# Performance work log

Hardware: AMD Instinct MI355X
Metric: run time of the kernel (lower is better)

The kernel has to match this reference:

```python
import jax, jax.numpy as jnp
import numpy as np

TOP_K = 64
TEMPERATURE = 1.0
EPS = 1e-12  # torch F.normalize eps


def _normalize(v):
    # matches torch.nn.functional.normalize(v, dim=-1)
    n = jnp.linalg.norm(v, axis=-1, keepdims=True)
    return v / jnp.maximum(n, EPS)


def setup_inputs() -> dict:
    key = jax.random.key(0)
    k1, k2 = jax.random.split(key)
    x = jax.random.normal(k1, (4, 1024, 768), dtype=jnp.float32)
    codebook = jax.random.normal(k2, (8192, 768), dtype=jnp.float32)
    alpha = jnp.float32(0.5)
    return {"x": x, "codebook": codebook, "alpha": alpha}


def reference(x, codebook, alpha):
    K = TOP_K
    x_n = _normalize(x)                              # [B,T,D]
    cb_n = _normalize(codebook)                      # [N,D]
    sims = jnp.einsum('btd,nd->btn', x_n, cb_n)      # [B,T,N]
    activations = jax.nn.relu(sims)
    topk_vals, topk_idx = jax.lax.top_k(activations, K)  # [B,T,K]
    protos = codebook[topk_idx]                      # [B,T,K,D] gather
    protos_n = _normalize(protos)
    # per-token KxK pairwise similarity
    sim = jnp.einsum('btkd,btjd->btkj', protos_n, protos_n)
    sim = sim - jnp.eye(K, dtype=sim.dtype)
    sim = jax.nn.relu(sim)
    w = jax.nn.softmax(topk_vals / TEMPERATURE, axis=-1)  # [B,T,K]
    inhibition = jnp.einsum('btkj,btj->btk', sim, w)      # [B,T,K]
    result_topk = jax.nn.relu(topk_vals * (1.0 - alpha * inhibition))
    out = jnp.einsum('btk,btkd->btd', result_topk, protos)  # weighted sum
    return x + out
```

## Files before the change

kernel.cpp:

```cpp
#include <hip/hip_runtime.h>

#define TOKENS 4096
#define DIM    768
#define NCODE  8192
#define TOPK   64
#define CAP    384
#define LCAP   24
#define TAU    0.07f
#define NBIN   256
#define SELCAP 128
#define POOL   80
#define BLO    61
#define BHI    67

typedef __attribute__((ext_vector_type(4))) float          f32x4;
typedef __attribute__((ext_vector_type(8))) _Float16       half8;
typedef __attribute__((ext_vector_type(8))) unsigned short ushort8;
typedef __attribute__((ext_vector_type(16))) signed char   c8x16;
typedef __attribute__((ext_vector_type(8)))  signed char   c8x8;

__device__ __forceinline__ unsigned short f2h(float f) {
  _Float16 h = (_Float16)f;
  return *(unsigned short*)&h;
}
__device__ __forceinline__ float h2f(unsigned short u) {
  _Float16 h = *(_Float16*)&u;
  return (float)h;
}

__device__ __forceinline__ int binof(float v) {
  int b = (int)((v - TAU) * (256.0f / 0.28f));
  return b < 0 ? 0 : (b > 255 ? 255 : b);
}

__device__ __forceinline__ void gload16(const unsigned short* g, unsigned short* l) {
  __builtin_amdgcn_global_load_lds((const __attribute__((address_space(1))) unsigned int*)g,
                                   (__attribute__((address_space(3))) unsigned int*)l,
                                   16, 0, 0);
}

__device__ __forceinline__ double dot12(const float4& xa, const float4& xb, const float4& xc,
                                        const float4& a, const float4& b, const float4& c) {
  double acc = (double)xa.x * (double)a.x;
  acc = fma((double)xa.y, (double)a.y, acc);
  acc = fma((double)xa.z, (double)a.z, acc);
  acc = fma((double)xa.w, (double)a.w, acc);
  acc = fma((double)xb.x, (double)b.x, acc);
  acc = fma((double)xb.y, (double)b.y, acc);
  acc = fma((double)xb.z, (double)b.z, acc);
  acc = fma((double)xb.w, (double)b.w, acc);
  acc = fma((double)xc.x, (double)c.x, acc);
  acc = fma((double)xc.y, (double)c.y, acc);
  acc = fma((double)xc.z, (double)c.z, acc);
  acc = fma((double)xc.w, (double)c.w, acc);
  return acc;
}

__global__ __launch_bounds__(256) void normcvt_kernel(const float* __restrict__ X,
                                                      const float* __restrict__ CB,
                                                      unsigned short* __restrict__ Xn,
                                                      unsigned short* __restrict__ CBn,
                                                      signed char* __restrict__ CBq,
                                                      float* __restrict__ scs,
                                                      double* __restrict__ rxd,
                                                      double* __restrict__ rcd) {
  int row = blockIdx.x, tid = threadIdx.x;
  bool isCB = row >= TOKENS;
  int lrow = isCB ? row - TOKENS : row;
  const float* v = (isCB ? CB : X) + (size_t)lrow * DIM;
  float a = v[tid], b = v[tid + 256], c = v[tid + 512];
  double s = (double)a * a + (double)b * b + (double)c * c;
#pragma unroll
  for (int off = 32; off > 0; off >>= 1) s += __shfl_xor(s, off);
  __shared__ double red[4];
  __shared__ float s_rf, s_qs;
  __shared__ float redm[4];
  if ((tid & 63) == 0) red[tid >> 6] = s;
  __syncthreads();
  if (tid == 0) {
    double t = red[0] + red[1] + red[2] + red[3];
    double r = 1.0 / fmax(sqrt(t), 1e-12);
    (isCB ? rcd : rxd)[lrow] = r;
    s_rf = (float)r;
  }
  __syncthreads();
  float rf = s_rf;
  float na = a * rf, nb = b * rf, nc = c * rf;
  unsigned short* o = (isCB ? CBn : Xn) + (size_t)lrow * DIM;
  o[tid]       = f2h(na);
  o[tid + 256] = f2h(nb);
  o[tid + 512] = f2h(nc);
  if (isCB) {
    float m = fmaxf(fabsf(na), fmaxf(fabsf(nb), fabsf(nc)));
#pragma unroll
    for (int off = 32; off > 0; off >>= 1) m = fmaxf(m, __shfl_xor(m, off));
    if ((tid & 63) == 0) redm[tid >> 6] = m;
    __syncthreads();
    if (tid == 0) {
      float M = fmaxf(fmaxf(redm[0], redm[1]), fmaxf(redm[2], redm[3]));
      M = fmaxf(M, 1e-8f);
      s_qs = 127.0f / M;
      scs[lrow] = M / 127.0f;
    }
    __syncthreads();
    float qs = s_qs;
    signed char* q = CBq + (size_t)lrow * DIM;
    int qa = (int)rintf(na * qs); qa = qa > 127 ? 127 : (qa < -127 ? -127 : qa);
    int qb = (int)rintf(nb * qs); qb = qb > 127 ? 127 : (qb < -127 ? -127 : qb);
    int qc = (int)rintf(nc * qs); qc = qc > 127 ? 127 : (qc < -127 ? -127 : qc);
    q[tid]       = (signed char)qa;
    q[tid + 256] = (signed char)qb;
    q[tid + 512] = (signed char)qc;
  }
}

__global__ __launch_bounds__(256, 4) void cand_gemm(const unsigned short* __restrict__ Xn,
                                                    const unsigned short* __restrict__ CBn,
                                                    int* __restrict__ cnt,
                                                    float* __restrict__ cval,
                                                    unsigned short* __restrict__ cidx) {
  __shared__ __attribute__((aligned(16))) unsigned short As[2][128 * 32];
  __shared__ __attribute__((aligned(16))) unsigned short Bs[2][128 * 32];
  int tid = threadIdx.x;

  int bid = blockIdx.x;
  int xcd = bid & 7;
  int pos = bid >> 3;
  int sr  = pos >> 6;
  int rr  = pos & 63;
  int mt  = sr * 8 + (rr & 7);
  int nt  = xcd * 8 + (rr >> 3);
  int bm = mt * 128, bn = nt * 128;

  int wave = tid >> 6, lane = tid & 63;
  int wm = (wave >> 1) * 64, wn = (wave & 1) * 64;
  int col = lane & 15, q = lane >> 4;

  int scol = (((lane & 3) ^ ((lane >> 2) & 3)) * 8);
  const unsigned short* gA0 = Xn  + (size_t)(bm + wave * 32 + (lane >> 2)) * DIM + scol;
  const unsigned short* gB0 = CBn + (size_t)(bn + wave * 32 + (lane >> 2)) * DIM + scol;
  int lofs = wave * 32 * 32;

  f32x4 acc[4][4];
#pragma unroll
  for (int mi = 0; mi < 4; ++mi)
#pragma unroll
    for (int ni = 0; ni < 4; ++ni) acc[mi][ni] = (f32x4){0.f, 0.f, 0.f, 0.f};

#pragma unroll
  for (int j = 0; j < 2; ++j) {
    gload16(gA0 + (size_t)(j * 16) * DIM, &As[0][lofs + j * 16 * 32]);
    gload16(gB0 + (size_t)(j * 16) * DIM, &Bs[0][lofs + j * 16 * 32]);
  }

  int rsw = (q ^ (col & 3)) * 8;
  for (int it = 0; it < 24; ++it) {
    int cur = it & 1, nxt = cur ^ 1;
    __syncthreads();
    if (it < 23) {
      int k1 = (it + 1) * 32;
#pragma unroll
      for (int j = 0; j < 2; ++j) {
        gload16(gA0 + (size_t)(j * 16) * DIM + k1, &As[nxt][lofs + j * 16 * 32]);
        gload16(gB0 + (size_t)(j * 16) * DIM + k1, &Bs[nxt][lofs + j * 16 * 32]);
      }
    }
    half8 af[4], bf[4];
#pragma unroll
    for (int mi = 0; mi < 4; ++mi)
      af[mi] = *(const half8*)&As[cur][(wm + mi * 16 + col) * 32 + rsw];
#pragma unroll
    for (int ni = 0; ni < 4; ++ni)
      bf[ni] = *(const half8*)&Bs[cur][(wn + ni * 16 + col) * 32 + rsw];
#pragma unroll
    for (int mi = 0; mi < 4; ++mi)
#pragma unroll
      for (int ni = 0; ni < 4; ++ni)
        acc[mi][ni] = __builtin_amdgcn_mfma_f32_16x16x32_f16(af[mi], bf[ni], acc[mi][ni], 0, 0, 0);
  }
  __syncthreads();

  float* lv            = (float*)&As[0][0];
  unsigned short* lid  = (unsigned short*)&Bs[0][0];
  int* lcnt            = (int*)((char*)&Bs[0][0] + 128 * LCAP * 2);
  int* lbase           = lcnt + 128;
  if (tid < 128) lcnt[tid] = 0;
  __syncthreads();
#pragma unroll
  for (int mi = 0; mi < 4; ++mi)
#pragma unroll
    for (int rg = 0; rg < 4; ++rg) {
      int ml = wm + mi * 16 + q * 4 + rg;
#pragma unroll
      for (int ni = 0; ni < 4; ++ni) {
        float val = acc[mi][ni][rg];
        if (val > TAU) {
          int n = bn + wn + ni * 16 + col;
          int s = atomicAdd(&lcnt[ml], 1);
          if (s < LCAP) { lv[ml * LCAP + s] = val; lid[ml * LCAP + s] = (unsigned short)n; }
        }
      }
    }
  __syncthreads();

  if (tid < 128) {
    int c = lcnt[tid]; c = c < LCAP ? c : LCAP;
    lcnt[tid] = c;
    lbase[tid] = atomicAdd(&cnt[bm + tid], c);
  }
  __syncthreads();
  {
    int ml = tid >> 1, half = tid & 1;
    int c = lcnt[ml], base = lbase[ml], m = bm + ml;
    for (int s = half; s < c; s += 2) {
      int g = base + s;
      if (g < CAP) {
        cval[(size_t)m * CAP + g] = lv[ml * LCAP + s];
        cidx[(size_t)m * CAP + g] = lid[ml * LCAP + s];
      }
    }
  }
}

__global__ __launch_bounds__(128) void select_kernel(const float* __restrict__ X,
                                                     const float* __restrict__ CB,
                                                     const double* __restrict__ rxd,
                                                     const double* __restrict__ rcd,
                                                     const int* __restrict__ cnt,
                                                     const float* __restrict__ cval,
                                                     const unsigned short* __restrict__ cidx,
                                                     unsigned short* __restrict__ gidx,
                                                     float* __restrict__ gvals) {
  int t = blockIdx.x, tid = threadIdx.x;
  int wave = tid >> 6, lane = tid & 63;

  __shared__ float  s_cv[CAP];
  __shared__ int    s_cid[CAP];
  __shared__ int    hist[NBIN];
  __shared__ float  s_selv[SELCAP];
  __shared__ int    s_seli[SELCAP];
  __shared__ float  s_ordv[POOL];
  __shared__ int    s_ord[POOL];
  __shared__ double s_bex[BHI - BLO];
  __shared__ int    s_idx[64];
  __shared__ float  s_vals[64];
  __shared__ int    s_n, s_pivot;

  int c = cnt[t]; c = c < CAP ? c : CAP;
  for (int s = tid; s < c; s += 128) {
    s_cv[s]  = cval[(size_t)t * CAP + s];
    s_cid[s] = (int)cidx[(size_t)t * CAP + s];
  }
  hist[tid] = 0;
  hist[tid + 128] = 0;
  if (tid == 0) s_n = 0;
  __syncthreads();
  for (int s = tid; s < c; s += 128) atomicAdd(&hist[binof(s_cv[s])], 1);
  __syncthreads();

  int target = c < POOL ? c : POOL;
  if (wave == 0) {
    int h0 = hist[4 * lane], h1 = hist[4 * lane + 1], h2 = hist[4 * lane + 2], h3 = hist[4 * lane + 3];
    int T = h0 + h1 + h2 + h3;
#pragma unroll
    for (int off = 1; off < 64; off <<= 1) {
      int x = __shfl_down(T, off);
      T += (lane + off < 64) ? x : 0;
    }
    int s0 = T, s1 = T - h0, s2 = s1 - h1, s3 = s2 - h2;
    int bk = -1;
    if (s3 >= target) bk = 3;
    else if (s2 >= target) bk = 2;
    else if (s1 >= target) bk = 1;
    else if (s0 >= target) bk = 0;
    unsigned long long m = __ballot(bk >= 0);
    int hl = 63 - __builtin_clzll(m);
    if (lane == hl) s_pivot = 4 * lane + bk;
  }
  __syncthreads();
  int pivot = s_pivot;
  for (int s = tid; s < c; s += 128) {
    if (binof(s_cv[s]) >= pivot) {
      int p = atomicAdd(&s_n, 1);
      if (p < SELCAP) { s_selv[p] = s_cv[s]; s_seli[p] = s_cid[s]; }
    }
  }
  __syncthreads();
  int nsel = s_n < SELCAP ? s_n : SELCAP;

  if (tid < nsel) {
    float vi = s_selv[tid]; int ci = s_seli[tid];
    int rank = 0;
    for (int j = 0; j < nsel; ++j) {
      float vj = s_selv[j]; int cj = s_seli[j];
      rank += (vj > vi || (vj == vi && cj < ci)) ? 1 : 0;
    }
    if (rank < POOL) { s_ord[rank] = ci; s_ordv[rank] = vi; }
  }
  if (tid < 64) { s_vals[tid] = 0.0f; s_idx[tid] = 0; }
  __syncthreads();

  int nord = nsel < POOL ? nsel : POOL;
  int lo = nord < BLO ? nord : BLO;
  int hi = nord < BHI ? nord : BHI;
  int B  = hi - lo;

  float4 xa = *(const float4*)(X + (size_t)t * DIM + 4 * lane);
  float4 xb = *(const float4*)(X + (size_t)t * DIM + 256 + 4 * lane);
  float4 xc = *(const float4*)(X + (size_t)t * DIM + 512 + 4 * lane);
  double rxt = rxd[t];
  for (int j = wave * 2; j < B; j += 4) {
    int r1ok = (j + 1) < B;
    int gi0 = s_ord[lo + j];
    int gi1 = r1ok ? s_ord[lo + j + 1] : gi0;
    const float* p0 = CB + (size_t)gi0 * DIM;
    const float* p1 = CB + (size_t)gi1 * DIM;
    float4 a0 = *(const float4*)(p0 + 4 * lane);
    float4 b0 = *(const float4*)(p0 + 256 + 4 * lane);
    float4 c0 = *(const float4*)(p0 + 512 + 4 * lane);
    float4 a1 = *(const float4*)(p1 + 4 * lane);
    float4 b1 = *(const float4*)(p1 + 256 + 4 * lane);
    float4 c1 = *(const float4*)(p1 + 512 + 4 * lane);
    double acc0 = dot12(xa, xb, xc, a0, b0, c0);
    double acc1 = dot12(xa, xb, xc, a1, b1, c1);
#pragma unroll
    for (int off = 32; off > 0; off >>= 1) {
      acc0 += __shfl_xor(acc0, off);
      acc1 += __shfl_xor(acc1, off);
    }
    if (lane == 0) {
      double v0 = acc0 * rxt * rcd[gi0];
      s_bex[j] = v0 > 0.0 ? v0 : 0.0;
      if (r1ok) {
        double v1 = acc1 * rxt * rcd[gi1];
        s_bex[j + 1] = v1 > 0.0 ? v1 : 0.0;
      }
    }
  }
  __syncthreads();

  if (tid < lo) { s_idx[tid] = s_ord[tid]; s_vals[tid] = s_ordv[tid]; }
  if (tid < B) {
    double vi = s_bex[tid]; int ci = s_ord[lo + tid];
    int rb = 0;
    for (int j = 0; j < B; ++j) {
      double vj = s_bex[j]; int cj = s_ord[lo + j];
      rb += (vj > vi || (vj == vi && cj < ci)) ? 1 : 0;
    }
    int slot = lo + rb;
    if (slot < TOPK) { s_idx[slot] = ci; s_vals[slot] = (float)vi; }
  }
  __syncthreads();

  if (tid < 64) {
    gidx[(size_t)t * 64 + tid]  = (unsigned short)s_idx[tid];
    gvals[(size_t)t * 64 + tid] = s_vals[tid];
  }
}

__global__ __launch_bounds__(256) void gram_kernel(const float* __restrict__ X,
                                                   const signed char* __restrict__ CBq,
                                                   const float* __restrict__ scs,
                                                   const double* __restrict__ rcd,
                                                   const unsigned short* __restrict__ gidx,
                                                   const float* __restrict__ gvals,
                                                   const float* __restrict__ alpha_p,
                                                   float* __restrict__ OUT) {
  int t = blockIdx.x, tid = threadIdx.x;
  int wave = tid >> 6, lane = tid & 63;

  __shared__ __attribute__((aligned(16))) unsigned char u_mem[17408];
  unsigned short (*Pb)[136] = (unsigned short (*)[136])u_mem;

  __shared__ int   s_idx[64];
  __shared__ float s_vals[64], s_w[64], s_rn[64], s_res[64];

  if (tid < 64) {
    s_idx[tid]  = (int)gidx[(size_t)t * 64 + tid];
    s_vals[tid] = gvals[(size_t)t * 64 + tid];
  }
  __syncthreads();

  if (tid < 64) {
    float v = s_vals[tid];
    float m = v;
#pragma unroll
    for (int off = 32; off > 0; off >>= 1) m = fmaxf(m, __shfl_xor(m, off));
    float e = expf(v - m);
    float se = e;
#pragma unroll
    for (int off = 32; off > 0; off >>= 1) se += __shfl_xor(se, off);
    s_w[tid] = e / se;
  }

  int q = lane >> 4, col = lane & 15;
  int frow = wave * 16 + col;
  int kof  = q * 8;
  f32x4 gacc[4];
#pragma unroll
  for (int cj = 0; cj < 4; ++cj) gacc[cj] = (f32x4){0.f, 0.f, 0.f, 0.f};
  int r = tid >> 2, qq = tid & 3;
  const signed char* Pg = CBq + (size_t)s_idx[r] * DIM;
  c8x16 stq[2];
  stq[0] = *(const c8x16*)(Pg + qq * 32);
  stq[1] = *(const c8x16*)(Pg + qq * 32 + 16);
  for (int cch = 0; cch < 6; ++cch) {
    if (cch) __syncthreads();
#pragma unroll
    for (int j = 0; j < 4; ++j) {
      ushort8 w;
#pragma unroll
      for (int e = 0; e < 8; ++e) w[e] = f2h((float)stq[j >> 1][(j & 1) * 8 + e]);
      *(ushort8*)&Pb[r][qq * 32 + j * 8] = w;
    }
    __syncthreads();
    if (cch < 5) {
      stq[0] = *(const c8x16*)(Pg + (cch + 1) * 128 + qq * 32);
      stq[1] = *(const c8x16*)(Pg + (cch + 1) * 128 + qq * 32 + 16);
    }
#pragma unroll
    for (int ks = 0; ks < 4; ++ks) {
      half8 a = *(const half8*)&Pb[frow][ks * 32 + kof];
#pragma unroll
      for (int cj = 0; cj < 4; ++cj) {
        half8 b = *(const half8*)&Pb[cj * 16 + col][ks * 32 + kof];
        gacc[cj] = __builtin_amdgcn_mfma_f32_16x16x32_f16(a, b, gacc[cj], 0, 0, 0);
      }
    }
  }

#pragma unroll
  for (int cj = 0; cj < 4; ++cj) {
    if (cj == wave) {
#pragma unroll
      for (int rg = 0; rg < 4; ++rg) {
        if (col == q * 4 + rg)
          s_rn[wave * 16 + q * 4 + rg] =
              1.0f / fmaxf(sqrtf(fmaxf(gacc[cj][rg], 0.0f)), 1e-12f);
      }
    }
  }
  __syncthreads();

  float alpha = alpha_p[0];
  {
    float inh[4] = {0.f, 0.f, 0.f, 0.f};
#pragma unroll
    for (int rg = 0; rg < 4; ++rg) {
      int i = wave * 16 + q * 4 + rg;
      float rni = s_rn[i];
#pragma unroll
      for (int cj = 0; cj < 4; ++cj) {
        int jcol = cj * 16 + col;
        if (jcol != i) {
          float sim = fmaxf(gacc[cj][rg] * rni * s_rn[jcol], 0.0f);
          inh[rg] += sim * s_w[jcol];
        }
      }
    }
#pragma unroll
    for (int off = 1; off < 16; off <<= 1) {
#pragma unroll
      for (int rg = 0; rg < 4; ++rg) inh[rg] += __shfl_xor(inh[rg], off);
    }
    if (col == 0) {
#pragma unroll
      for (int rg = 0; rg < 4; ++rg) {
        int i = wave * 16 + q * 4 + rg;
        int gi = s_idx[i];
        float res = s_vals[i] * (1.0f - alpha * inh[rg]);
        s_res[i] = fmaxf(res, 0.0f) * scs[gi] * (float)(1.0 / rcd[gi]);
      }
    }
  }
  __syncthreads();

  float* s_o  = (float*)u_mem;
  float* s_p1 = s_o + DIM;
  {
    float o8[8];
#pragma unroll
    for (int j = 0; j < 8; ++j) o8[j] = 0.f;
    int wr = tid / 96, wc = tid - wr * 96;
    if (wr < 2) {
      const int d8 = wc * 8;
#pragma unroll 8
      for (int i = 0; i < 32; ++i) {
        int k = 2 * i + wr;
        float rk = s_res[k];
        const signed char* p = CBq + (size_t)s_idx[k] * DIM + d8;
        c8x8 v = *(const c8x8*)p;
#pragma unroll
        for (int j = 0; j < 8; ++j) o8[j] += rk * (float)v[j];
      }
    }
    if (wr == 1) {
#pragma unroll
      for (int j = 0; j < 8; ++j) s_p1[wc * 8 + j] = o8[j];
    }
    __syncthreads();
    if (wr == 0) {
#pragma unroll
      for (int j = 0; j < 8; ++j) s_o[wc * 8 + j] = o8[j] + s_p1[wc * 8 + j];
    }
    __syncthreads();
  }

  OUT[(size_t)t * DIM + tid]       = X[(size_t)t * DIM + tid]       + s_o[tid];
  OUT[(size_t)t * DIM + tid + 256] = X[(size_t)t * DIM + tid + 256] + s_o[tid + 256];
  OUT[(size_t)t * DIM + tid + 512] = X[(size_t)t * DIM + tid + 512] + s_o[tid + 512];
}

extern "C" void kernel_launch(void* const* d_in, const int* in_sizes, int n_in,
                              void* d_out, int out_size, void* d_ws, size_t ws_size,
                              hipStream_t stream) {
  const float* X       = (const float*)d_in[0];
  const float* CB      = (const float*)d_in[1];
  const float* alpha_p = (const float*)d_in[2];
  float* OUT = (float*)d_out;

  double* rxd          = (double*)d_ws;
  double* rcd          = rxd + TOKENS;
  int*    cnt          = (int*)(rcd + NCODE);
  float*  cval         = (float*)(cnt + TOKENS);
  unsigned short* cidx = (unsigned short*)(cval + (size_t)TOKENS * CAP);
  unsigned short* Xn   = cidx + (size_t)TOKENS * CAP;
  unsigned short* CBn  = Xn + (size_t)TOKENS * DIM;
  signed char*    CBq  = (signed char*)(CBn + (size_t)NCODE * DIM);
  float*          scs  = (float*)(CBq + (size_t)NCODE * DIM);
  unsigned short* gidx = (unsigned short*)(scs + NCODE);
  float*          gvals= (float*)(gidx + (size_t)TOKENS * 64);

  hipMemsetAsync(cnt, 0, TOKENS * sizeof(int), stream);
  hipLaunchKernelGGL(normcvt_kernel, dim3(TOKENS + NCODE), dim3(256), 0, stream,
                     X, CB, Xn, CBn, CBq, scs, rxd, rcd);
  hipLaunchKernelGGL(cand_gemm, dim3(2048), dim3(256), 0, stream,
                     Xn, CBn, cnt, cval, cidx);
  hipLaunchKernelGGL(select_kernel, dim3(TOKENS), dim3(128), 0, stream,
                     X, CB, rxd, rcd, cnt, cval, cidx, gidx, gvals);
  hipLaunchKernelGGL(gram_kernel, dim3(TOKENS), dim3(256), 0, stream,
                     X, CBq, scs, rcd, gidx, gvals, alpha_p, OUT);
}
```

Before: 256.6 us.

## Switch candidate similarity GEMM from fp16 to int8 MFMA with per-row scales

The candidate-screening GEMM now quantizes both normalized tokens and codebook rows to int8 with per-row scales and uses the i32 16x16x64 int8 MFMA, halving operand bytes and doubling K per instruction. The normalization kernel fuses the max-abs reduction with the norm reduction and writes int8 directly instead of fp16. Because int8 similarities are coarser, the exact-refinement bin window BLO/BHI is widened, which may send more candidates into the select stage's exact recheck. The LDS layout drops the XOR swizzle, which risks bank conflicts.

```diff
diff --git a/kernel.cpp b/kernel.cpp
--- a/kernel.cpp
+++ b/kernel.cpp
@@ -10,10 +10,11 @@
 #define NBIN   256
 #define SELCAP 128
 #define POOL   80
-#define BLO    61
-#define BHI    67
+#define BLO    49
+#define BHI    79
 
 typedef __attribute__((ext_vector_type(4))) float          f32x4;
+typedef __attribute__((ext_vector_type(4))) int            i32x4;
 typedef __attribute__((ext_vector_type(8))) _Float16       half8;
 typedef __attribute__((ext_vector_type(8))) unsigned short ushort8;
 typedef __attribute__((ext_vector_type(16))) signed char   c8x16;
@@ -23,17 +24,13 @@
   _Float16 h = (_Float16)f;
   return *(unsigned short*)&h;
 }
-__device__ __forceinline__ float h2f(unsigned short u) {
-  _Float16 h = *(_Float16*)&u;
-  return (float)h;
-}
 
 __device__ __forceinline__ int binof(float v) {
   int b = (int)((v - TAU) * (256.0f / 0.28f));
   return b < 0 ? 0 : (b > 255 ? 255 : b);
 }
 
-__device__ __forceinline__ void gload16(const unsigned short* g, unsigned short* l) {
+__device__ __forceinline__ void gload16(const void* g, void* l) {
   __builtin_amdgcn_global_load_lds((const __attribute__((address_space(1))) unsigned int*)g,
                                    (__attribute__((address_space(3))) unsigned int*)l,
                                    16, 0, 0);
@@ -58,9 +55,9 @@
 
 __global__ __launch_bounds__(256) void normcvt_kernel(const float* __restrict__ X,
                                                       const float* __restrict__ CB,
-                                                      unsigned short* __restrict__ Xn,
-                                                      unsigned short* __restrict__ CBn,
+                                                      signed char* __restrict__ Xq,
                                                       signed char* __restrict__ CBq,
+                                                      float* __restrict__ sxq,
                                                       float* __restrict__ scs,
                                                       double* __restrict__ rxd,
                                                       double* __restrict__ rcd) {
@@ -70,57 +67,45 @@
   const float* v = (isCB ? CB : X) + (size_t)lrow * DIM;
   float a = v[tid], b = v[tid + 256], c = v[tid + 512];
   double s = (double)a * a + (double)b * b + (double)c * c;
-#pragma unroll
-  for (int off = 32; off > 0; off >>= 1) s += __shfl_xor(s, off);
+  float m = fmaxf(fabsf(a), fmaxf(fabsf(b), fabsf(c)));
+#pragma unroll
+  for (int off = 32; off > 0; off >>= 1) {
+    s += __shfl_xor(s, off);
+    m = fmaxf(m, __shfl_xor(m, off));
+  }
   __shared__ double red[4];
-  __shared__ float s_rf, s_qs;
   __shared__ float redm[4];
-  if ((tid & 63) == 0) red[tid >> 6] = s;
+  __shared__ float s_qs;
+  if ((tid & 63) == 0) { red[tid >> 6] = s; redm[tid >> 6] = m; }
   __syncthreads();
   if (tid == 0) {
     double t = red[0] + red[1] + red[2] + red[3];
     double r = 1.0 / fmax(sqrt(t), 1e-12);
     (isCB ? rcd : rxd)[lrow] = r;
-    s_rf = (float)r;
-  }
-  __syncthreads();
-  float rf = s_rf;
-  float na = a * rf, nb = b * rf, nc = c * rf;
-  unsigned short* o = (isCB ? CBn : Xn) + (size_t)lrow * DIM;
-  o[tid]       = f2h(na);
-  o[tid + 256] = f2h(nb);
-  o[tid + 512] = f2h(nc);
-  if (isCB) {
-    float m = fmaxf(fabsf(na), fmaxf(fabsf(nb), fabsf(nc)));
-#pragma unroll
-    for (int off = 32; off > 0; off >>= 1) m = fmaxf(m, __shfl_xor(m, off));
-    if ((tid & 63) == 0) redm[tid >> 6] = m;
-    __syncthreads();
-    if (tid == 0) {
-      float M = fmaxf(fmaxf(redm[0], redm[1]), fmaxf(redm[2], redm[3]));
-      M = fmaxf(M, 1e-8f);
-      s_qs = 127.0f / M;
-      scs[lrow] = M / 127.0f;
-    }
-    __syncthreads();
-    float qs = s_qs;
-    signed char* q = CBq + (size_t)lrow * DIM;
-    int qa = (int)rintf(na * qs); qa = qa > 127 ? 127 : (qa < -127 ? -127 : qa);
-    int qb = (int)rintf(nb * qs); qb = qb > 127 ? 127 : (qb < -127 ? -127 : qb);
-    int qc = (int)rintf(nc * qs); qc = qc > 127 ? 127 : (qc < -127 ? -127 : qc);
-    q[tid]       = (signed char)qa;
-    q[tid + 256] = (signed char)qb;
-    q[tid + 512] = (signed char)qc;
-  }
-}
-
-__global__ __launch_bounds__(256, 4) void cand_gemm(const unsigned short* __restrict__ Xn,
-                                                    const unsigned short* __restrict__ CBn,
+    float Mn = fmaxf((float)r * fmaxf(fmaxf(redm[0], redm[1]), fmaxf(redm[2], redm[3])), 1e-8f);
+    s_qs = 127.0f / Mn * (float)r;
+    (isCB ? scs : sxq)[lrow] = Mn / 127.0f;
+  }
+  __syncthreads();
+  float qs = s_qs;
+  signed char* o = (isCB ? CBq : Xq) + (size_t)lrow * DIM;
+  int qa = (int)rintf(a * qs); qa = qa > 127 ? 127 : (qa < -127 ? -127 : qa);
+  int qb = (int)rintf(b * qs); qb = qb > 127 ? 127 : (qb < -127 ? -127 : qb);
+  int qc = (int)rintf(c * qs); qc = qc > 127 ? 127 : (qc < -127 ? -127 : qc);
+  o[tid]       = (signed char)qa;
+  o[tid + 256] = (signed char)qb;
+  o[tid + 512] = (signed char)qc;
+}
+
+__global__ __launch_bounds__(256, 4) void cand_gemm(const signed char* __restrict__ Xq,
+                                                    const signed char* __restrict__ CBq,
+                                                    const float* __restrict__ sxq,
+                                                    const float* __restrict__ scs,
                                                     int* __restrict__ cnt,
                                                     float* __restrict__ cval,
                                                     unsigned short* __restrict__ cidx) {
-  __shared__ __attribute__((aligned(16))) unsigned short As[2][128 * 32];
-  __shared__ __attribute__((aligned(16))) unsigned short Bs[2][128 * 32];
+  __shared__ __attribute__((aligned(16))) signed char As[2][128 * 64];
+  __shared__ __attribute__((aligned(16))) signed char Bs[2][128 * 64];
   int tid = threadIdx.x;
 
   int bid = blockIdx.x;
@@ -136,64 +121,66 @@
   int wm = (wave >> 1) * 64, wn = (wave & 1) * 64;
   int col = lane & 15, q = lane >> 4;
 
-  int scol = (((lane & 3) ^ ((lane >> 2) & 3)) * 8);
-  const unsigned short* gA0 = Xn  + (size_t)(bm + wave * 32 + (lane >> 2)) * DIM + scol;
-  const unsigned short* gB0 = CBn + (size_t)(bn + wave * 32 + (lane >> 2)) * DIM + scol;
-  int lofs = wave * 32 * 32;
-
-  f32x4 acc[4][4];
+  const signed char* gA0 = Xq  + (size_t)(bm + wave * 32 + (lane >> 2)) * DIM + (lane & 3) * 16;
+  const signed char* gB0 = CBq + (size_t)(bn + wave * 32 + (lane >> 2)) * DIM + (lane & 3) * 16;
+  int lofs = wave * 32 * 64;
+
+  i32x4 acc[4][4];
 #pragma unroll
   for (int mi = 0; mi < 4; ++mi)
 #pragma unroll
-    for (int ni = 0; ni < 4; ++ni) acc[mi][ni] = (f32x4){0.f, 0.f, 0.f, 0.f};
+    for (int ni = 0; ni < 4; ++ni) acc[mi][ni] = (i32x4){0, 0, 0, 0};
 
 #pragma unroll
   for (int j = 0; j < 2; ++j) {
-    gload16(gA0 + (size_t)(j * 16) * DIM, &As[0][lofs + j * 16 * 32]);
-    gload16(gB0 + (size_t)(j * 16) * DIM, &Bs[0][lofs + j * 16 * 32]);
-  }
-
-  int rsw = (q ^ (col & 3)) * 8;
-  for (int it = 0; it < 24; ++it) {
+    gload16(gA0 + (size_t)(j * 16) * DIM, &As[0][lofs + j * 16 * 64]);
+    gload16(gB0 + (size_t)(j * 16) * DIM, &Bs[0][lofs + j * 16 * 64]);
+  }
+
+  for (int it = 0; it < 12; ++it) {
     int cur = it & 1, nxt = cur ^ 1;
     __syncthreads();
-    if (it < 23) {
-      int k1 = (it + 1) * 32;
+    if (it < 11) {
+      int k1 = (it + 1) * 64;
 #pragma unroll
       for (int j = 0; j < 2; ++j) {
-        gload16(gA0 + (size_t)(j * 16) * DIM + k1, &As[nxt][lofs + j * 16 * 32]);
-        gload16(gB0 + (size_t)(j * 16) * DIM + k1, &Bs[nxt][lofs + j * 16 * 32]);
-      }
-    }
-    half8 af[4], bf[4];
+        gload16(gA0 + (size_t)(j * 16) * DIM + k1, &As[nxt][lofs + j * 16 * 64]);
+        gload16(gB0 + (size_t)(j * 16) * DIM + k1, &Bs[nxt][lofs + j * 16 * 64]);
+      }
+    }
+    i32x4 af[4], bf[4];
 #pragma unroll
     for (int mi = 0; mi < 4; ++mi)
-      af[mi] = *(const half8*)&As[cur][(wm + mi * 16 + col) * 32 + rsw];
+      af[mi] = *(const i32x4*)&As[cur][(wm + mi * 16 + col) * 64 + q * 16];
 #pragma unroll
     for (int ni = 0; ni < 4; ++ni)
-      bf[ni] = *(const half8*)&Bs[cur][(wn + ni * 16 + col) * 32 + rsw];
+      bf[ni] = *(const i32x4*)&Bs[cur][(wn + ni * 16 + col) * 64 + q * 16];
 #pragma unroll
     for (int mi = 0; mi < 4; ++mi)
 #pragma unroll
       for (int ni = 0; ni < 4; ++ni)
-        acc[mi][ni] = __builtin_amdgcn_mfma_f32_16x16x32_f16(af[mi], bf[ni], acc[mi][ni], 0, 0, 0);
+        acc[mi][ni] = __builtin_amdgcn_mfma_i32_16x16x64_i8(af[mi], bf[ni], acc[mi][ni], 0, 0, 0);
   }
   __syncthreads();
 
   float* lv            = (float*)&As[0][0];
   unsigned short* lid  = (unsigned short*)&Bs[0][0];
-  int* lcnt            = (int*)((char*)&Bs[0][0] + 128 * LCAP * 2);
+  int* lcnt            = (int*)(&Bs[0][0] + 128 * LCAP * 2);
   int* lbase           = lcnt + 128;
   if (tid < 128) lcnt[tid] = 0;
   __syncthreads();
+  float sn[4];
+#pragma unroll
+  for (int ni = 0; ni < 4; ++ni) sn[ni] = scs[bn + wn + ni * 16 + col];
 #pragma unroll
   for (int mi = 0; mi < 4; ++mi)
 #pragma unroll
     for (int rg = 0; rg < 4; ++rg) {
       int ml = wm + mi * 16 + q * 4 + rg;
+      float sm = sxq[bm + ml];
 #pragma unroll
       for (int ni = 0; ni < 4; ++ni) {
-        float val = acc[mi][ni][rg];
+        float val = (float)acc[mi][ni][rg] * sm * sn[ni];
         if (val > TAU) {
           int n = bn + wn + ni * 16 + col;
           int s = atomicAdd(&lcnt[ml], 1);
@@ -524,18 +511,18 @@
   int*    cnt          = (int*)(rcd + NCODE);
   float*  cval         = (float*)(cnt + TOKENS);
   unsigned short* cidx = (unsigned short*)(cval + (size_t)TOKENS * CAP);
-  unsigned short* Xn   = cidx + (size_t)TOKENS * CAP;
-  unsigned short* CBn  = Xn + (size_t)TOKENS * DIM;
-  signed char*    CBq  = (signed char*)(CBn + (size_t)NCODE * DIM);
-  float*          scs  = (float*)(CBq + (size_t)NCODE * DIM);
+  signed char*    Xq   = (signed char*)(cidx + (size_t)TOKENS * CAP);
+  signed char*    CBq  = Xq + (size_t)TOKENS * DIM;
+  float*          sxq  = (float*)(CBq + (size_t)NCODE * DIM);
+  float*          scs  = sxq + TOKENS;
   unsigned short* gidx = (unsigned short*)(scs + NCODE);
   float*          gvals= (float*)(gidx + (size_t)TOKENS * 64);
 
   hipMemsetAsync(cnt, 0, TOKENS * sizeof(int), stream);
   hipLaunchKernelGGL(normcvt_kernel, dim3(TOKENS + NCODE), dim3(256), 0, stream,
-                     X, CB, Xn, CBn, CBq, scs, rxd, rcd);
+                     X, CB, Xq, CBq, sxq, scs, rxd, rcd);
   hipLaunchKernelGGL(cand_gemm, dim3(2048), dim3(256), 0, stream,
-                     Xn, CBn, cnt, cval, cidx);
+                     Xq, CBq, sxq, scs, cnt, cval, cidx);
   hipLaunchKernelGGL(select_kernel, dim3(TOKENS), dim3(128), 0, stream,
                      X, CB, rxd, rcd, cnt, cval, cidx, gidx, gvals);
   hipLaunchKernelGGL(gram_kernel, dim3(TOKENS), dim3(256), 0, stream,
```

Measured after the change: 272.3 us. 6.1% more time.
